# Kernel optimization log

Hardware: AMD Instinct MI355X
Metric: run time of the kernel (lower is better)

Reference implementation:

```python
import jax, jax.numpy as jnp
import numpy as np

B, T, V, E, D = 64, 512, 512, 128, 256


def setup_inputs() -> dict:
    key = jax.random.key(0)
    ks = jax.random.split(key, 9)
    g = lambda k, sh, s: jax.random.normal(k, sh, jnp.float32) * np.float32(s)
    return {
        "x": jax.random.randint(ks[0], (B, T), 0, V),
        "embed": g(ks[1], (V, E), 1.0),
        "W_ih": g(ks[2], (E, D), 1.0 / np.sqrt(E)),
        "W_hh": g(ks[3], (D, D), 1.0 / np.sqrt(D)),
        "b_h": jnp.zeros((D,), jnp.float32),
        "W_attn": g(ks[4], (D, D), 1.0 / np.sqrt(D)),
        "U_attn": g(ks[5], (D, D), 1.0 / np.sqrt(D)),
        "v_attn": g(ks[6], (D,), 1.0 / np.sqrt(D)),
        "fc_W": g(ks[7], (2 * D, V), 1.0 / np.sqrt(2 * D)),
        "fc_b": jnp.zeros((V,), jnp.float32),
    }


def _forward(x, embed, W_ih, W_hh, b_h, W_attn, U_attn, v_attn, fc_W, fc_b):
    Bn, Tn = x.shape
    Dn = W_hh.shape[0]
    # precompute input projection for every step: [T, B, D]
    xp = jnp.swapaxes(embed[x] @ W_ih + b_h, 0, 1)
    pos = jnp.arange(Tn)

    def step(carry, x_t):
        h_prev, Hbuf, Pbuf, t = carry  # Hbuf: past hidden states, Pbuf: W_attn-projected
        h = jnp.tanh(x_t + h_prev @ W_hh)  # [B, D]
        # Bahdanau attention over strictly-past states (slots < t)
        cur_proj = h @ U_attn  # [B, D]
        energy = jnp.einsum('tbd,d->tb', jnp.tanh(Pbuf + cur_proj[None]), v_attn)
        energy = jnp.where((pos < t)[:, None], energy, -1e9)
        w = jax.nn.softmax(energy, axis=0)  # [T, B]
        ctx = jnp.einsum('tb,tbd->bd', w, Hbuf)
        ctx = jnp.where(t == 0, h, ctx)  # first step: context = h itself
        logits = jnp.concatenate([h, ctx], axis=-1) @ fc_W + fc_b  # [B, V]
        Hbuf = Hbuf.at[t].set(h)
        Pbuf = Pbuf.at[t].set(h @ W_attn)
        return (h, Hbuf, Pbuf, t + 1), logits

    h0 = jnp.zeros((Bn, Dn), xp.dtype)
    buf = jnp.zeros((Tn, Bn, Dn), xp.dtype)
    _, outs = jax.lax.scan(step, (h0, buf, buf, jnp.asarray(0, jnp.int32)), xp)
    return jnp.swapaxes(outs, 0, 1)  # [B, T, V]


def reference(x, embed, W_ih, W_hh, b_h, W_attn, U_attn, v_attn, fc_W, fc_b):
    return _forward(x, embed, W_ih, W_hh, b_h, W_attn, U_attn, v_attn, fc_W, fc_b)
```

## Files before the change

### kernel.cpp

```cpp
#include <hip/hip_runtime.h>
#include <hip/hip_bf16.h>

#define B_  64
#define T_  512
#define V_  512
#define E_  128
#define D_  256
#define D2_ 512

typedef unsigned short u16;
typedef unsigned int   u32;
typedef short s16x8 __attribute__((ext_vector_type(8)));
typedef _Float16 f16x8 __attribute__((ext_vector_type(8)));
typedef float f32x4 __attribute__((ext_vector_type(4)));
typedef unsigned short u16x2 __attribute__((ext_vector_type(2)));
typedef unsigned short u16x4 __attribute__((ext_vector_type(4)));

__device__ __forceinline__ float bf2f(u16 u){
    union { u32 i; float f; } c; c.i = ((u32)u) << 16; return c.f;
}
__device__ __forceinline__ u16 f2bf(float f){
    union { float f; u32 i; } c; c.f = f;
    u32 u = c.i;
    return (u16)((u + 0x7fffu + ((u >> 16) & 1u)) >> 16);
}
__device__ __forceinline__ u16 f2h(float f){
    union { _Float16 h; u16 u; } c; c.h = (_Float16)f; return c.u;
}
__device__ __forceinline__ float tanh_b(float x){
    float e = __expf(2.0f * x);
    return fmaf(-2.0f, __builtin_amdgcn_rcpf(e + 1.0f), 1.0f);
}
__device__ __forceinline__ void barrier_lgkm(){
    asm volatile("s_waitcnt lgkmcnt(0)\n\ts_barrier" ::: "memory");
}

__global__ __launch_bounds__(256) void k_ew(const float* __restrict__ embed,
                                            const float* __restrict__ W_ih,
                                            const float* __restrict__ b_h,
                                            float* __restrict__ EW){
    __shared__ float er[E_];
    int v = blockIdx.x;
    int tid = threadIdx.x;
    if (tid < E_) er[tid] = embed[v*E_ + tid];
    __syncthreads();
    float acc = b_h[tid];
    #pragma unroll 4
    for (int e = 0; e < E_; ++e) acc += er[e] * W_ih[e*D_ + tid];
    EW[v*D_ + tid] = acc;
}

__global__ __launch_bounds__(256) void k_gather(const int* __restrict__ x,
                                                const float* __restrict__ EW,
                                                float* __restrict__ XP){
    int m = blockIdx.x * 4 + (threadIdx.x >> 6);
    int lane = threadIdx.x & 63;
    int b = m & 63, t = m >> 6;
    int v = x[b*T_ + t];
    float4 val = *(const float4*)&EW[v*D_ + lane*4];
    *(float4*)&XP[(size_t)m*D_ + lane*4] = val;
}

__global__ __launch_bounds__(256) void k_cvt(const float* __restrict__ W,
                                             u16* __restrict__ Wb,
                                             int N, int K){
    int i = blockIdx.x * 256 + threadIdx.x;
    int n = i / K, k = i - n*K;
    Wb[(size_t)n*K + k] = f2bf(W[(size_t)k*N + n]);
}

__global__ __launch_bounds__(512, 2) void k_rnn(const float* __restrict__ XP,
                                                const float* __restrict__ W_hh,
                                                u16* __restrict__ HC){
    __shared__ u16 hf[2][4][272];
    int tid  = threadIdx.x;
    int lane = tid & 63;
    int w    = tid >> 6;
    int col  = lane & 15;
    int colA = col & 3;
    int quad = lane >> 4;
    int bb0  = blockIdx.x * 4;

    f16x8 bfh[2][8];
    #pragma unroll
    for (int nt = 0; nt < 2; ++nt){
        int n = w*32 + nt*16 + col;
        #pragma unroll
        for (int ks = 0; ks < 8; ++ks){
            f16x8 th;
            #pragma unroll
            for (int j = 0; j < 8; ++j){
                int k = ks*32 + quad*8 + j;
                th[j] = (_Float16)W_hh[k*D_ + n];
            }
            bfh[nt][ks] = th;
        }
    }
    for (int i = tid; i < 2*4*272; i += 512) (&hf[0][0][0])[i] = 0;

    const float* p  = XP + (size_t)bb0*D_ + w*32 + col;
    u16*         hc = HC + (size_t)bb0*D2_ + w*32 + col;

    float ewv[2][4];
    #pragma unroll
    for (int nt = 0; nt < 2; ++nt)
        #pragma unroll
        for (int r = 0; r < 4; ++r)
            ewv[nt][r] = p[r*D_ + nt*16];
    p += (size_t)B_*D_;
    __syncthreads();

    for (int t = 0; t < T_; ++t){
        int rb = t & 1, wb = rb ^ 1;
        f32x4 acc[2];
        #pragma unroll
        for (int nt = 0; nt < 2; ++nt)
            #pragma unroll
            for (int r = 0; r < 4; ++r) acc[nt][r] = ewv[nt][r];

        f16x8 ah[8];
        #pragma unroll
        for (int ks = 0; ks < 8; ++ks)
            ah[ks] = *(const f16x8*)&hf[rb][colA][ks*32 + quad*8];

        if (t + 1 < T_){
            #pragma unroll
            for (int nt = 0; nt < 2; ++nt)
                #pragma unroll
                for (int r = 0; r < 4; ++r)
                    ewv[nt][r] = p[r*D_ + nt*16];
        }
        p += (size_t)B_*D_;

        #pragma unroll
        for (int ks = 0; ks < 8; ++ks){
            acc[0] = __builtin_amdgcn_mfma_f32_16x16x32_f16(ah[ks], bfh[0][ks], acc[0], 0, 0, 0);
            acc[1] = __builtin_amdgcn_mfma_f32_16x16x32_f16(ah[ks], bfh[1][ks], acc[1], 0, 0, 0);
        }

        #pragma unroll
        for (int nt = 0; nt < 2; ++nt){
            f32x4 s = acc[nt];
            float v = (quad & 2) ? ((quad & 1) ? s[3] : s[2])
                                 : ((quad & 1) ? s[1] : s[0]);
            float h  = tanh_b(v);
            int n    = w*32 + nt*16 + col;
            hf[wb][quad][n]      = f2h(h);
            hc[quad*D2_ + nt*16] = f2bf(h);
        }
        hc += (size_t)B_*D2_;
        barrier_lgkm();
    }
}

__global__ __launch_bounds__(256) void k_gemm(const u16* __restrict__ A, int lda,
                                              const u16* __restrict__ Wb,
                                              const float* __restrict__ bias,
                                              void* __restrict__ out,
                                              int K, int N, int mode){
    __shared__ u16 As[64][88];
    __shared__ u16 Ws[64][88];
    int tid  = threadIdx.x;
    int lane = tid & 63;
    int w    = tid >> 6;
    int col  = lane & 15;
    int quad = lane >> 4;
    int m0   = blockIdx.x * 64;
    int n0   = blockIdx.y * 64;

    f32x4 acc[4];
    #pragma unroll
    for (int nt = 0; nt < 4; ++nt)
        #pragma unroll
        for (int r = 0; r < 4; ++r) acc[nt][r] = 0.0f;

    for (int kk = 0; kk < K; kk += 64){
        #pragma unroll
        for (int i = 0; i < 2; ++i){
            int idx = tid + i*256;
            int r   = idx >> 3;
            int c8  = (idx & 7) * 8;
            *(s16x8*)&As[r][c8] = *(const s16x8*)&A [(size_t)(m0 + r)*lda + kk + c8];
            *(s16x8*)&Ws[r][c8] = *(const s16x8*)&Wb[(size_t)(n0 + r)*K   + kk + c8];
        }
        barrier_lgkm();
        #pragma unroll
        for (int ks = 0; ks < 2; ++ks){
            s16x8 a = *(const s16x8*)&As[w*16 + col][ks*32 + quad*8];
            #pragma unroll
            for (int nt = 0; nt < 4; ++nt){
                s16x8 b = *(const s16x8*)&Ws[nt*16 + col][ks*32 + quad*8];
                acc[nt] = __builtin_amdgcn_mfma_f32_16x16x32_bf16(a, b, acc[nt], 0, 0, 0);
            }
        }
        barrier_lgkm();
    }
    #pragma unroll
    for (int nt = 0; nt < 4; ++nt){
        int n = n0 + nt*16 + col;
        float bv = (mode == 1 && bias) ? bias[n] : 0.0f;
        #pragma unroll
        for (int r = 0; r < 4; ++r){
            int m = m0 + w*16 + quad*4 + r;
            float v = acc[nt][r] + bv;
            if (mode == 1){
                int b = m & 63, t = m >> 6;
                ((float*)out)[(size_t)(b*T_ + t)*V_ + n] = v;
            } else if (mode == 2){
                ((u16*)out)[(size_t)m*N + n] = f2bf(__expf(2.0f * v));
            } else if (mode == 3){
                u16* dst = (u16*)out + ((size_t)(n >> 8)) * ((size_t)32768 * 256);
                dst[(size_t)m*256 + (n & 255)] = f2bf(__expf(2.0f * v));
            } else {
                ((u16*)out)[(size_t)m*N + n] = f2bf(v);
            }
        }
    }
}

__global__ __launch_bounds__(512) void k_fc(const u16* __restrict__ A,
                                            const u16* __restrict__ Wb,
                                            const float* __restrict__ bias,
                                            float* __restrict__ out){
    __shared__ u16 As[128][88];
    __shared__ u16 Ws[128][88];
    int tid  = threadIdx.x;
    int lane = tid & 63;
    int w    = tid >> 6;
    int wm   = w >> 2;
    int wn   = w & 3;
    int col  = lane & 15;
    int quad = lane >> 4;
    int m0   = blockIdx.x * 128;
    int n0   = blockIdx.y * 128;

    f32x4 acc[4][2];
    #pragma unroll
    for (int mt = 0; mt < 4; ++mt)
        #pragma unroll
        for (int nt = 0; nt < 2; ++nt)
            #pragma unroll
            for (int r = 0; r < 4; ++r) acc[mt][nt][r] = 0.0f;

    for (int kk = 0; kk < D2_; kk += 64){
        #pragma unroll
        for (int i = 0; i < 2; ++i){
            int idx = tid + i*512;
            int r   = idx >> 3;
            int c8  = (idx & 7) * 8;
            *(s16x8*)&As[r][c8] = *(const s16x8*)&A [(size_t)(m0 + r)*D2_ + kk + c8];
            *(s16x8*)&Ws[r][c8] = *(const s16x8*)&Wb[(size_t)(n0 + r)*D2_ + kk + c8];
        }
        barrier_lgkm();
        #pragma unroll
        for (int ks = 0; ks < 2; ++ks){
            s16x8 b0 = *(const s16x8*)&Ws[wn*32 +      col][ks*32 + quad*8];
            s16x8 b1 = *(const s16x8*)&Ws[wn*32 + 16 + col][ks*32 + quad*8];
            #pragma unroll
            for (int mt = 0; mt < 4; ++mt){
                s16x8 a = *(const s16x8*)&As[wm*64 + mt*16 + col][ks*32 + quad*8];
                acc[mt][0] = __builtin_amdgcn_mfma_f32_16x16x32_bf16(a, b0, acc[mt][0], 0, 0, 0);
                acc[mt][1] = __builtin_amdgcn_mfma_f32_16x16x32_bf16(a, b1, acc[mt][1], 0, 0, 0);
            }
        }
        barrier_lgkm();
    }
    #pragma unroll
    for (int nt = 0; nt < 2; ++nt){
        int n = n0 + wn*32 + nt*16 + col;
        float bv = bias[n];
        #pragma unroll
        for (int mt = 0; mt < 4; ++mt){
            #pragma unroll
            for (int r = 0; r < 4; ++r){
                int m = m0 + wm*64 + mt*16 + quad*4 + r;
                int b = m & 63, t = m >> 6;
                out[(size_t)(b*T_ + t)*V_ + n] = acc[mt][nt][r] + bv;
            }
        }
    }
}

__global__ __launch_bounds__(256) void k_energy(const u16* __restrict__ EP,
                                                const u16* __restrict__ EQ,
                                                const float* __restrict__ v_attn,
                                                u16* __restrict__ Wx,
                                                float* __restrict__ l){
    __shared__ float eps[32][288];
    int tid = threadIdx.x;
    int blk = blockIdx.x;
    int b   = blk / 136;
    int pi  = blk % 136;
    int tt  = 0;
    while ((tt+1)*(tt+2)/2 <= pi) ++tt;
    int pt  = pi - tt*(tt+1)/2;

    int t_l = tid >> 3;
    int dg  = tid & 7;
    int d0  = dg * 32;
    int t   = tt*32 + t_l;

    #pragma unroll
    for (int i = 0; i < 8; ++i){
        int idx = tid + i*256;
        int row = idx >> 6;
        int c4  = (idx & 63) * 4;
        int pc  = c4 + ((c4 >> 5) << 2);
        u16x4 v4 = *(const u16x4*)&EP[((size_t)((pt*32 + row)*B_ + b))*D_ + c4];
        float4 f4 = make_float4(bf2f(v4.x), bf2f(v4.y), bf2f(v4.z), bf2f(v4.w));
        *(float4*)&eps[row][pc] = f4;
    }

    float eq[32], vm2[32], sv = 0.0f;
    #pragma unroll
    for (int i = 0; i < 8; ++i){
        u16x4 v4 = *(const u16x4*)&EQ[((size_t)(t*B_ + b))*D_ + d0 + i*4];
        eq[i*4+0] = bf2f(v4.x); eq[i*4+1] = bf2f(v4.y);
        eq[i*4+2] = bf2f(v4.z); eq[i*4+3] = bf2f(v4.w);
    }
    #pragma unroll
    for (int i = 0; i < 32; ++i){
        float v = v_attn[d0 + i];
        sv += v;
        vm2[i] = -2.0f * v;
    }
    barrier_lgkm();

    float lsum = 0.0f;
    for (int tpl = 0; tpl < 32; ++tpl){
        int tp = pt*32 + tpl;
        float acc = sv;
        #pragma unroll
        for (int g = 0; g < 8; ++g){
            float4 ep = *(const float4*)&eps[tpl][dg*36 + 4*g];
            float da = fmaf(ep.x, eq[4*g+0], 1.0f);
            float db = fmaf(ep.y, eq[4*g+1], 1.0f);
            float dc = fmaf(ep.z, eq[4*g+2], 1.0f);
            float dd = fmaf(ep.w, eq[4*g+3], 1.0f);
            float dab = da * db;
            float dcd = dc * dd;
            float nab = fmaf(vm2[4*g+1], da, vm2[4*g+0] * db);
            float ncd = fmaf(vm2[4*g+3], dc, vm2[4*g+2] * dd);
            float num = fmaf(ncd, dab, nab * dcd);
            acc = fmaf(num, __builtin_amdgcn_rcpf(dab * dcd), acc);
        }
        acc += __shfl_xor(acc, 1);
        acc += __shfl_xor(acc, 2);
        acc += __shfl_xor(acc, 4);
        float pe = __expf(acc);
        if (dg == 0 && tp < t){
            u16 peb = f2bf(pe);
            Wx[((size_t)(b*T_ + t))*T_ + tp] = peb;
            lsum += bf2f(peb);
        }
    }
    if (dg == 0 && lsum != 0.0f) atomicAdd(&l[b*T_ + t], lsum);
}

__global__ __launch_bounds__(256) void k_ctx(const u16* __restrict__ Wx,
                                             u16* __restrict__ HC,
                                             const float* __restrict__ l){
    __shared__ u16 As[64][88];
    __shared__ u16 Ws[64][88];
    int tid  = threadIdx.x;
    int lane = tid & 63;
    int w    = tid >> 6;
    int col  = lane & 15;
    int quad = lane >> 4;
    int b    = blockIdx.y;
    int m0   = (blockIdx.x >> 2) * 64;
    int n0   = (blockIdx.x & 3) * 64;

    const u16* A = Wx + (size_t)b * T_ * T_;

    f32x4 acc[4];
    #pragma unroll
    for (int nt = 0; nt < 4; ++nt)
        #pragma unroll
        for (int r = 0; r < 4; ++r) acc[nt][r] = 0.0f;

    int kmax = m0 + 64;
    for (int kk = 0; kk < kmax; kk += 64){
        #pragma unroll
        for (int i = 0; i < 2; ++i){
            int idx = tid + i*256;
            int r   = idx >> 3;
            int c8  = (idx & 7) * 8;
            *(s16x8*)&As[r][c8] = *(const s16x8*)&A[(size_t)(m0 + r)*T_ + kk + c8];
        }
        #pragma unroll
        for (int i = 0; i < 8; ++i){
            int idx = tid + i*256;
            int k   = idx >> 5;
            int n2  = (idx & 31) * 2;
            u16x2 v2 = *(const u16x2*)&HC[((size_t)((kk + k)*B_ + b))*D2_ + n0 + n2];
            Ws[n2][k]   = v2.x;
            Ws[n2+1][k] = v2.y;
        }
        barrier_lgkm();
        #pragma unroll
        for (int ks = 0; ks < 2; ++ks){
            s16x8 a = *(const s16x8*)&As[w*16 + col][ks*32 + quad*8];
            #pragma unroll
            for (int nt = 0; nt < 4; ++nt){
                s16x8 bb = *(const s16x8*)&Ws[nt*16 + col][ks*32 + quad*8];
                acc[nt] = __builtin_amdgcn_mfma_f32_16x16x32_bf16(a, bb, acc[nt], 0, 0, 0);
            }
        }
        barrier_lgkm();
    }

    float linv[4];
    #pragma unroll
    for (int r = 0; r < 4; ++r){
        int t = m0 + w*16 + quad*4 + r;
        float lv = (t > 0) ? l[b*T_ + t] : 1.0f;
        linv[r] = 1.0f / lv;
    }
    #pragma unroll
    for (int nt = 0; nt < 4; ++nt){
        int n = n0 + nt*16 + col;
        #pragma unroll
        for (int r = 0; r < 4; ++r){
            int t = m0 + w*16 + quad*4 + r;
            u16 ov;
            if (t == 0) ov = HC[(size_t)b*D2_ + n];
            else        ov = f2bf(acc[nt][r] * linv[r]);
            HC[((size_t)(t*B_ + b))*D2_ + D_ + n] = ov;
        }
    }
}

extern "C" void kernel_launch(void* const* d_in, const int* in_sizes, int n_in,
                              void* d_out, int out_size, void* d_ws, size_t ws_size,
                              hipStream_t stream){
    const int*   x     = (const int*)d_in[0];
    const float* embed = (const float*)d_in[1];
    const float* W_ih  = (const float*)d_in[2];
    const float* W_hh  = (const float*)d_in[3];
    const float* b_h   = (const float*)d_in[4];
    const float* W_att = (const float*)d_in[5];
    const float* U_att = (const float*)d_in[6];
    const float* v_att = (const float*)d_in[7];
    const float* fc_W  = (const float*)d_in[8];
    const float* fc_b  = (const float*)d_in[9];

    char* ws = (char*)d_ws;
    float* EW   = (float*)ws;
    u16*   fcWb = (u16*)ws;
    u16*   HC   = (u16*)(ws + 524288);
    u16*   EP   = (u16*)(ws + 34078720);
    u16*   EQ   = (u16*)(ws + 50855936);
    float* XP   = (float*)(ws + 34078720);
    float* l    = (float*)(ws + 67633152);
    u16*   Wab  = (u16*)(ws + 67764224);
    u16*   Uab  = (u16*)(ws + 67895296);
    u16*   Wx   = (u16*)d_out;

    (void)hipMemsetAsync(d_out, 0, (size_t)B_*T_*T_*2, stream);
    (void)hipMemsetAsync(l, 0, B_*T_*4, stream);

    k_ew    <<<dim3(V_),          dim3(256), 0, stream>>>(embed, W_ih, b_h, EW);
    k_gather<<<dim3(T_*B_/4),     dim3(256), 0, stream>>>(x, EW, XP);
    k_cvt   <<<dim3(D_*D_/256),   dim3(256), 0, stream>>>(W_att, Wab, D_, D_);
    k_cvt   <<<dim3(D_*D_/256),   dim3(256), 0, stream>>>(U_att, Uab, D_, D_);
    k_cvt   <<<dim3(D2_*V_/256),  dim3(256), 0, stream>>>(fc_W, fcWb, V_, D2_);
    k_rnn   <<<dim3(16),          dim3(512), 0, stream>>>(XP, W_hh, HC);
    k_gemm  <<<dim3(512, 8),      dim3(256), 0, stream>>>(HC, D2_, Wab, nullptr, (void*)EP, D_, D2_, 3);
    k_energy<<<dim3(B_*136),      dim3(256), 0, stream>>>(EP, EQ, v_att, Wx, l);
    k_ctx   <<<dim3(32, B_),      dim3(256), 0, stream>>>(Wx, HC, l);
    k_fc    <<<dim3(256, 4),      dim3(512), 0, stream>>>(HC, fcWb, fc_b, (float*)d_out);
}
```

Before: 702.7 us.

## Fuse weight conversions, split RNN MFMA chains, tile energy over two query steps

Three separate changes. The three transpose-convert launches are merged into one kernel. The recurrent MFMA accumulation is split into two independent chains that are summed before tanh, which shortens the serial dependency on the critical per-step path. The energy kernel now has each thread handle two query timesteps, so each shared-memory key tile is reused twice and the grid shrinks to 72 blocks per batch, at the cost of higher register pressure and coarser triangular tiles that may add masked work.

After: 719.1 us. +2.3%, slower.

```diff
diff --git a/kernel.cpp b/kernel.cpp
--- a/kernel.cpp
+++ b/kernel.cpp
@@ -61,12 +61,25 @@
     *(float4*)&XP[(size_t)m*D_ + lane*4] = val;
 }
 
-__global__ __launch_bounds__(256) void k_cvt(const float* __restrict__ W,
-                                             u16* __restrict__ Wb,
-                                             int N, int K){
+__global__ __launch_bounds__(256) void k_cvt3(const float* __restrict__ W_att,
+                                              const float* __restrict__ U_att,
+                                              const float* __restrict__ fc_W,
+                                              u16* __restrict__ Wab,
+                                              u16* __restrict__ Uab,
+                                              u16* __restrict__ fcWb){
     int i = blockIdx.x * 256 + threadIdx.x;
-    int n = i / K, k = i - n*K;
-    Wb[(size_t)n*K + k] = f2bf(W[(size_t)k*N + n]);
+    if (i < 65536){
+        int n = i >> 8, k = i & 255;
+        Wab[i] = f2bf(W_att[k*D_ + n]);
+    } else if (i < 131072){
+        int j = i - 65536;
+        int n = j >> 8, k = j & 255;
+        Uab[j] = f2bf(U_att[k*D_ + n]);
+    } else {
+        int j = i - 131072;
+        int n = j >> 9, k = j & 511;
+        fcWb[j] = f2bf(fc_W[k*V_ + n]);
+    }
 }
 
 __global__ __launch_bounds__(512, 2) void k_rnn(const float* __restrict__ XP,
@@ -112,11 +125,11 @@
 
     for (int t = 0; t < T_; ++t){
         int rb = t & 1, wb = rb ^ 1;
-        f32x4 acc[2];
+        f32x4 accA[2], accB[2];
         #pragma unroll
         for (int nt = 0; nt < 2; ++nt)
             #pragma unroll
-            for (int r = 0; r < 4; ++r) acc[nt][r] = ewv[nt][r];
+            for (int r = 0; r < 4; ++r){ accA[nt][r] = ewv[nt][r]; accB[nt][r] = 0.0f; }
 
         f16x8 ah[8];
         #pragma unroll
@@ -133,17 +146,21 @@
         p += (size_t)B_*D_;
 
         #pragma unroll
-        for (int ks = 0; ks < 8; ++ks){
-            acc[0] = __builtin_amdgcn_mfma_f32_16x16x32_f16(ah[ks], bfh[0][ks], acc[0], 0, 0, 0);
-            acc[1] = __builtin_amdgcn_mfma_f32_16x16x32_f16(ah[ks], bfh[1][ks], acc[1], 0, 0, 0);
+        for (int ks = 0; ks < 4; ++ks){
+            accA[0] = __builtin_amdgcn_mfma_f32_16x16x32_f16(ah[ks],   bfh[0][ks],   accA[0], 0, 0, 0);
+            accA[1] = __builtin_amdgcn_mfma_f32_16x16x32_f16(ah[ks],   bfh[1][ks],   accA[1], 0, 0, 0);
+            accB[0] = __builtin_amdgcn_mfma_f32_16x16x32_f16(ah[ks+4], bfh[0][ks+4], accB[0], 0, 0, 0);
+            accB[1] = __builtin_amdgcn_mfma_f32_16x16x32_f16(ah[ks+4], bfh[1][ks+4], accB[1], 0, 0, 0);
         }
 
         #pragma unroll
         for (int nt = 0; nt < 2; ++nt){
-            f32x4 s = acc[nt];
-            float v = (quad & 2) ? ((quad & 1) ? s[3] : s[2])
-                                 : ((quad & 1) ? s[1] : s[0]);
-            float h  = tanh_b(v);
+            f32x4 sA = accA[nt], sB = accB[nt];
+            float vA = (quad & 2) ? ((quad & 1) ? sA[3] : sA[2])
+                                  : ((quad & 1) ? sA[1] : sA[0]);
+            float vB = (quad & 2) ? ((quad & 1) ? sB[3] : sB[2])
+                                  : ((quad & 1) ? sB[1] : sB[0]);
+            float h  = tanh_b(vA + vB);
             int n    = w*32 + nt*16 + col;
             hf[wb][quad][n]      = f2h(h);
             hc[quad*D2_ + nt*16] = f2bf(h);
@@ -289,16 +306,16 @@
     __shared__ float eps[32][288];
     int tid = threadIdx.x;
     int blk = blockIdx.x;
-    int b   = blk / 136;
-    int pi  = blk % 136;
-    int tt  = 0;
-    while ((tt+1)*(tt+2)/2 <= pi) ++tt;
-    int pt  = pi - tt*(tt+1)/2;
-
-    int t_l = tid >> 3;
+    int b   = blk / 72;
+    int pi  = blk % 72;
+    int tm  = 0;
+    while ((tm+1)*(tm+2) <= pi) ++tm;
+    int pt  = pi - tm*(tm+1);
+
+    int tg  = tid >> 3;
     int dg  = tid & 7;
     int d0  = dg * 32;
-    int t   = tt*32 + t_l;
+    int t0  = tm*64 + tg*2;
 
     #pragma unroll
     for (int i = 0; i < 8; ++i){
@@ -311,12 +328,15 @@
         *(float4*)&eps[row][pc] = f4;
     }
 
-    float eq[32], vm2[32], sv = 0.0f;
+    float eq0[32], eq1[32], vm2[32], sv = 0.0f;
     #pragma unroll
     for (int i = 0; i < 8; ++i){
-        u16x4 v4 = *(const u16x4*)&EQ[((size_t)(t*B_ + b))*D_ + d0 + i*4];
-        eq[i*4+0] = bf2f(v4.x); eq[i*4+1] = bf2f(v4.y);
-        eq[i*4+2] = bf2f(v4.z); eq[i*4+3] = bf2f(v4.w);
+        u16x4 a4 = *(const u16x4*)&EQ[((size_t)(t0*B_ + b))*D_ + d0 + i*4];
+        u16x4 b4 = *(const u16x4*)&EQ[((size_t)((t0+1)*B_ + b))*D_ + d0 + i*4];
+        eq0[i*4+0] = bf2f(a4.x); eq0[i*4+1] = bf2f(a4.y);
+        eq0[i*4+2] = bf2f(a4.z); eq0[i*4+3] = bf2f(a4.w);
+        eq1[i*4+0] = bf2f(b4.x); eq1[i*4+1] = bf2f(b4.y);
+        eq1[i*4+2] = bf2f(b4.z); eq1[i*4+3] = bf2f(b4.w);
     }
     #pragma unroll
     for (int i = 0; i < 32; ++i){
@@ -326,35 +346,55 @@
     }
     barrier_lgkm();
 
-    float lsum = 0.0f;
+    float lsum0 = 0.0f, lsum1 = 0.0f;
     for (int tpl = 0; tpl < 32; ++tpl){
         int tp = pt*32 + tpl;
-        float acc = sv;
+        float a0 = sv, a1 = sv;
         #pragma unroll
         for (int g = 0; g < 8; ++g){
             float4 ep = *(const float4*)&eps[tpl][dg*36 + 4*g];
-            float da = fmaf(ep.x, eq[4*g+0], 1.0f);
-            float db = fmaf(ep.y, eq[4*g+1], 1.0f);
-            float dc = fmaf(ep.z, eq[4*g+2], 1.0f);
-            float dd = fmaf(ep.w, eq[4*g+3], 1.0f);
-            float dab = da * db;
-            float dcd = dc * dd;
-            float nab = fmaf(vm2[4*g+1], da, vm2[4*g+0] * db);
-            float ncd = fmaf(vm2[4*g+3], dc, vm2[4*g+2] * dd);
-            float num = fmaf(ncd, dab, nab * dcd);
-            acc = fmaf(num, __builtin_amdgcn_rcpf(dab * dcd), acc);
-        }
-        acc += __shfl_xor(acc, 1);
-        acc += __shfl_xor(acc, 2);
-        acc += __shfl_xor(acc, 4);
-        float pe = __expf(acc);
-        if (dg == 0 && tp < t){
-            u16 peb = f2bf(pe);
-            Wx[((size_t)(b*T_ + t))*T_ + tp] = peb;
-            lsum += bf2f(peb);
-        }
-    }
-    if (dg == 0 && lsum != 0.0f) atomicAdd(&l[b*T_ + t], lsum);
+            {
+                float da = fmaf(ep.x, eq0[4*g+0], 1.0f);
+                float db = fmaf(ep.y, eq0[4*g+1], 1.0f);
+                float dc = fmaf(ep.z, eq0[4*g+2], 1.0f);
+                float dd = fmaf(ep.w, eq0[4*g+3], 1.0f);
+                float dab = da * db, dcd = dc * dd;
+                float nab = fmaf(vm2[4*g+1], da, vm2[4*g+0] * db);
+                float ncd = fmaf(vm2[4*g+3], dc, vm2[4*g+2] * dd);
+                float num = fmaf(ncd, dab, nab * dcd);
+                a0 = fmaf(num, __builtin_amdgcn_rcpf(dab * dcd), a0);
+            }
+            {
+                float da = fmaf(ep.x, eq1[4*g+0], 1.0f);
+                float db = fmaf(ep.y, eq1[4*g+1], 1.0f);
+                float dc = fmaf(ep.z, eq1[4*g+2], 1.0f);
+                float dd = fmaf(ep.w, eq1[4*g+3], 1.0f);
+                float dab = da * db, dcd = dc * dd;
+                float nab = fmaf(vm2[4*g+1], da, vm2[4*g+0] * db);
+                float ncd = fmaf(vm2[4*g+3], dc, vm2[4*g+2] * dd);
+                float num = fmaf(ncd, dab, nab * dcd);
+                a1 = fmaf(num, __builtin_amdgcn_rcpf(dab * dcd), a1);
+            }
+        }
+        a0 += __shfl_xor(a0, 1); a0 += __shfl_xor(a0, 2); a0 += __shfl_xor(a0, 4);
+        a1 += __shfl_xor(a1, 1); a1 += __shfl_xor(a1, 2); a1 += __shfl_xor(a1, 4);
+        if (dg == 0){
+            if (tp < t0){
+                u16 peb = f2bf(__expf(a0));
+                Wx[((size_t)(b*T_ + t0))*T_ + tp] = peb;
+                lsum0 += bf2f(peb);
+            }
+            if (tp < t0 + 1){
+                u16 peb = f2bf(__expf(a1));
+                Wx[((size_t)(b*T_ + t0 + 1))*T_ + tp] = peb;
+                lsum1 += bf2f(peb);
+            }
+        }
+    }
+    if (dg == 0){
+        if (lsum0 != 0.0f) atomicAdd(&l[b*T_ + t0], lsum0);
+        if (lsum1 != 0.0f) atomicAdd(&l[b*T_ + t0 + 1], lsum1);
+    }
 }
 
 __global__ __launch_bounds__(256) void k_ctx(const u16* __restrict__ Wx,
@@ -462,12 +502,10 @@
 
     k_ew    <<<dim3(V_),          dim3(256), 0, stream>>>(embed, W_ih, b_h, EW);
     k_gather<<<dim3(T_*B_/4),     dim3(256), 0, stream>>>(x, EW, XP);
-    k_cvt   <<<dim3(D_*D_/256),   dim3(256), 0, stream>>>(W_att, Wab, D_, D_);
-    k_cvt   <<<dim3(D_*D_/256),   dim3(256), 0, stream>>>(U_att, Uab, D_, D_);
-    k_cvt   <<<dim3(D2_*V_/256),  dim3(256), 0, stream>>>(fc_W, fcWb, V_, D2_);
+    k_cvt3  <<<dim3(1536),        dim3(256), 0, stream>>>(W_att, U_att, fc_W, Wab, Uab, fcWb);
     k_rnn   <<<dim3(16),          dim3(512), 0, stream>>>(XP, W_hh, HC);
     k_gemm  <<<dim3(512, 8),      dim3(256), 0, stream>>>(HC, D2_, Wab, nullptr, (void*)EP, D_, D2_, 3);
-    k_energy<<<dim3(B_*136),      dim3(256), 0, stream>>>(EP, EQ, v_att, Wx, l);
+    k_energy<<<dim3(B_*72),       dim3(256), 0, stream>>>(EP, EQ, v_att, Wx, l);
     k_ctx   <<<dim3(32, B_),      dim3(256), 0, stream>>>(Wx, HC, l);
     k_fc    <<<dim3(256, 4),      dim3(512), 0, stream>>>(HC, fcWb, fc_b, (float*)d_out);
 }
```
